# Kernel tuning notes

Hardware: AMD Instinct MI355X
Metric: run time of the kernel (lower is better)

Reference implementation:

```python
import jax, jax.numpy as jnp
import numpy as np

# MANO fingertip / palm prior vertex indices from contact_loss
_F1 = [697,698,699,700,712,713,714,715,737,738,739,740,741,743,744,745,746,748,749,750,753,754,755,756,757,758,759,760,761,762,763,764,765,766,767,768]
_F2 = [46,47,48,49,164,165,166,167,194,195,223,237,238,280,281,298,301,317,320,323,324,325,326,327,328,329,330,331,332,333,340,341,342,343,344,345,346,347,348,349,350,351,352,353,354,355]
_F3 = [356,357,358,359,375,376,386,387,396,397,402,403,413,429,433,434,435,436,437,438,439,440,441,442,443,444,452,453,454,455,456,459,460,461,462,463,464,465,466,467]
_F4 = [468,469,470,471,484,485,486,496,497,506,507,513,514,524,545,546,547,548,549,550,551,552,553,555,563,564,565,566,567,570,572,573,574,575,576,577,578]
_F5 = [580,581,582,583,600,601,602,614,615,624,625,630,631,641,663,664,665,666,667,668,670,672,680,681,682,683,684,686,687,688,689,690,691,692,693,694,695]
_F0 = [73,96,98,99,772,774,775,777]
PRIOR_IDX = np.array(_F1 + _F2 + _F3 + _F4 + _F5 + _F0, dtype=np.int32)

KL_COEF = 0.005
A_W, B_W, C_W, D_W, E_W = 1.0, 0.1, 1000.0, 10.0, 10.0  # init kwargs a..e


def _nn(src, trg):
    """Brute-force 1-NN: src [B,N1,3] -> trg [B,N2,3].
    Returns (sq_dist [B,N1], idx [B,N1], diff src-near [B,N1,3])."""
    d2 = (jnp.sum(src * src, -1)[:, :, None]
          + jnp.sum(trg * trg, -1)[:, None, :]
          - 2.0 * jnp.einsum('bnd,bmd->bnm', src, trg))  # [B,N1,N2]
    idx = jnp.argmin(d2, axis=-1)
    near = jnp.take_along_axis(trg, idx[:, :, None], axis=1)
    diff = src - near
    return jnp.sum(diff * diff, axis=-1), idx, diff


def _p2p_signed(x, y, x_normals):
    """point2point_signed(x, y, x_normals): signed dist y->x, unsigned x->y."""
    _, yidx, y2x = _nn(y, x)  # nearest x for each y
    y_nn_normal = jnp.take_along_axis(x_normals, yidx[:, :, None], axis=1)
    in_out = jnp.sign(jnp.sum(y_nn_normal * y2x, axis=-1))
    y2x_signed = jnp.sqrt(jnp.sum(y2x * y2x, axis=-1)) * in_out  # [B,P2]
    _, _, x2y = _nn(x, y)  # nearest y for each x
    x2y_dist = jnp.sqrt(jnp.sum(x2y * x2y, axis=-1))  # [B,P1]
    return y2x_signed, x2y_dist


def _forward(recon_xyz, gt_xyz, recon_normals, gt_normals, obj_xyz, mean, log_var, v_weights):
    B = recon_xyz.shape[0]
    f32 = recon_xyz.dtype
    # --- CVAE recon (L2) + KLD ---
    recon_loss = jnp.sum((recon_xyz - gt_xyz) ** 2) / B
    kld = -0.5 * jnp.sum(1.0 + log_var - mean ** 2 - jnp.exp(log_var)) / B * 10.0
    # --- obj -> hand NN (squared dists, pytorch3d knn_points convention) ---
    recon_d2, recon_idx, _ = _nn(obj_xyz, recon_xyz)  # [B,3000]
    gt_d2, _, _ = _nn(obj_xyz, gt_xyz)
    # --- contact map from GT NN dist thresholding ---
    cmap = jnp.sqrt(gt_d2) < 0.005  # [B,3000] bool
    # --- contact_loss: obj NN to prior (fingertip/palm) recon verts ---
    prior = recon_xyz[:, PRIOR_IDX, :]
    obj_cd, _, _ = _nn(obj_xyz, prior)
    n_pts = jnp.sum(cmap.astype(f32))
    contact = 3000.0 * jnp.where(n_pts > 0, jnp.sum(obj_cd * cmap) / (B * n_pts), 0.0)
    # --- CMap_consistency_loss ---
    recon_cmap = jnp.sqrt(recon_d2) < 0.005
    consistency = -5.0 * jnp.sum((recon_cmap & cmap).astype(f32)) / (n_pts + 1e-4)
    # --- inter_penetr_loss: interior obj points via NN-normal dot sign ---
    nn_hand = jnp.take_along_axis(recon_xyz, recon_idx[:, :, None], axis=1)
    nn_normal = jnp.take_along_axis(recon_normals, recon_idx[:, :, None], axis=1)
    interior = jnp.sum((nn_hand - obj_xyz) * nn_normal, axis=-1) > 0
    penetr = 100.0 * jnp.sum(recon_d2 * interior) / B
    # --- loss_cnet: signed chamfer consistency ---
    vw2 = v_weights ** (1.0 / 2.5)
    o2h, h2o = _p2p_signed(recon_xyz, obj_xyz, recon_normals)
    o2h_gt, h2o_gt = _p2p_signed(gt_xyz, obj_xyz, gt_normals)
    w_dist = (o2h_gt < 0.01) & (o2h_gt > -0.005)
    w_neg = o2h < 0.0
    w = jnp.where(w_neg, 1.5, jnp.where(w_dist, 1.0, 0.1))
    loss_h = 35.0 * (1.0 - KL_COEF) * jnp.mean(jnp.abs(jnp.abs(h2o) - jnp.abs(h2o_gt)) * vw2)
    loss_o = 30.0 * (1.0 - KL_COEF) * jnp.mean(jnp.abs(o2h - o2h_gt) * w)
    cnet = loss_h + loss_o
    return (A_W * recon_loss + B_W * kld + C_W * penetr
            + D_W * contact + E_W * consistency + cnet)


def setup_inputs() -> dict:
    key = jax.random.key(0)
    ks = jax.random.split(key, 8)
    B, NH, NO, Z = 32, 778, 3000, 64
    s = 0.05  # meter-scale point clouds so contact thresholds (5mm) are meaningful
    def unit(k, shape):
        v = jax.random.normal(k, shape, dtype=jnp.float32)
        return v / jnp.linalg.norm(v, axis=-1, keepdims=True)
    return {
        'recon_xyz': jax.random.normal(ks[0], (B, NH, 3), dtype=jnp.float32) * s,
        'gt_xyz': jax.random.normal(ks[1], (B, NH, 3), dtype=jnp.float32) * s,
        'recon_normals': unit(ks[2], (B, NH, 3)),
        'gt_normals': unit(ks[3], (B, NH, 3)),
        'obj_xyz': jax.random.normal(ks[4], (B, NO, 3), dtype=jnp.float32) * s,
        'mean': jax.random.normal(ks[5], (B, Z), dtype=jnp.float32),
        'log_var': jax.random.normal(ks[6], (B, Z), dtype=jnp.float32) * 0.1,
        'v_weights': jax.random.uniform(ks[7], (NH,), dtype=jnp.float32),
    }


def reference(recon_xyz, gt_xyz, recon_normals, gt_normals, obj_xyz, mean, log_var, v_weights):
    return _forward(recon_xyz, gt_xyz, recon_normals, gt_normals, obj_xyz, mean, log_var, v_weights)
```

## Files before the change

kernel.cpp:

```cpp
#include <hip/hip_runtime.h>
#include <math.h>


#define NB 32
#define NH 778
#define NO 3000
#define NZ 64
#define NP 204

#define P_OBJ 4
#define OBJ_PTS (256 * P_OBJ)
#define OBJ_TILES 3
#define JSPLIT 4
#define JCH 195
#define OC_NUM 12
#define OC_SIZE 250

#define OBJ_BLKS (NB * OBJ_TILES * JSPLIT)
#define HAND_BLKS (NB * OC_NUM)
#define FIN_OBJ_BLKS (NB * OBJ_TILES)
#define FIN_TAIL_BLKS ((NB * NH + 255) / 256)
#define FIN_BLKS (FIN_OBJ_BLKS + FIN_TAIL_BLKS)

typedef unsigned int uint32;
typedef unsigned long long ull;

__device__ __constant__ int c_prior[NP] = {
  697,698,699,700,712,713,714,715,737,738,739,740,741,743,744,745,746,748,749,750,
  753,754,755,756,757,758,759,760,761,762,763,764,765,766,767,768,
  46,47,48,49,164,165,166,167,194,195,223,237,238,280,281,298,301,317,320,323,
  324,325,326,327,328,329,330,331,332,333,340,341,342,343,344,345,346,347,348,349,
  350,351,352,353,354,355,
  356,357,358,359,375,376,386,387,396,397,402,403,413,429,433,434,435,436,437,438,
  439,440,441,442,443,444,452,453,454,455,456,459,460,461,462,463,464,465,466,467,
  468,469,470,471,484,485,486,496,497,506,507,513,514,524,545,546,547,548,549,550,
  551,552,553,555,563,564,565,566,567,570,572,573,574,575,576,577,578,
  580,581,582,583,600,601,602,614,615,624,625,630,631,641,663,664,665,666,667,668,
  670,672,680,681,682,683,684,686,687,688,689,690,691,692,693,694,695,
  73,96,98,99,772,774,775,777
};

__device__ inline float wave_sum(float v) {
  v += __shfl_down(v, 32);
  v += __shfl_down(v, 16);
  v += __shfl_down(v, 8);
  v += __shfl_down(v, 4);
  v += __shfl_down(v, 2);
  v += __shfl_down(v, 1);
  return v;
}

#define N_MINH (2 * NB * NH)
#define N_PACK (2 * NB * NO)

__global__ void init_kernel(float* accs, uint32* minH, ull* packO) {
  int t = blockIdx.x * blockDim.x + threadIdx.x;
  if (t < 9) accs[t] = 0.0f;
  if (t < N_MINH) minH[t] = 0x7F800000u;
  if (t < N_PACK) packO[t] = ~0ull;
}

__global__ __launch_bounds__(256) void mega1(
    const float* __restrict__ recon, const float* __restrict__ gt,
    const float* __restrict__ obj,
    uint32* __restrict__ minHR, uint32* __restrict__ minHG,
    ull* __restrict__ packR, ull* __restrict__ packG)
{
  const int bid = blockIdx.x;
  const int tid = threadIdx.x;

  if (bid < OBJ_BLKS) {
    __shared__ float4 sR[JCH];
    __shared__ float4 sG[JCH];
    const int b    = bid / (OBJ_TILES * JSPLIT);
    const int rem  = bid % (OBJ_TILES * JSPLIT);
    const int tile = rem / JSPLIT;
    const int half = rem % JSPLIT;
    const int jbase = half * JCH;
    const int jcnt = (NH - jbase < JCH) ? (NH - jbase) : JCH;

    for (int i = tid; i < jcnt; i += 256) {
      const float* p = recon + ((size_t)b * NH + jbase + i) * 3;
      float x = p[0], y = p[1], z = p[2];
      sR[i] = make_float4(x, y, z, x*x + y*y + z*z);
      const float* q = gt + ((size_t)b * NH + jbase + i) * 3;
      float gx = q[0], gy = q[1], gz = q[2];
      sG[i] = make_float4(gx, gy, gz, gx*gx + gy*gy + gz*gz);
    }
    __syncthreads();

    float nx[P_OBJ], ny[P_OBJ], nz[P_OBJ], o2v[P_OBJ];
    int ob[P_OBJ]; bool val[P_OBJ];
    #pragma unroll
    for (int m = 0; m < P_OBJ; ++m) {
      int o = tile * OBJ_PTS + m * 256 + tid;
      ob[m] = o; val[m] = (o < NO);
      float x = 0.f, y = 0.f, z = 0.f;
      if (val[m]) {
        const float* op = obj + ((size_t)b * NO + o) * 3;
        x = op[0]; y = op[1]; z = op[2];
      }
      nx[m] = -2.f * x; ny[m] = -2.f * y; nz[m] = -2.f * z;
      o2v[m] = x*x + y*y + z*z;
    }

    float bR[P_OBJ], bG[P_OBJ]; int iR[P_OBJ], iG[P_OBJ];
    #pragma unroll
    for (int m = 0; m < P_OBJ; ++m) { bR[m] = 3.4e38f; bG[m] = 3.4e38f; iR[m] = 0; iG[m] = 0; }

    #pragma unroll 2
    for (int i = 0; i < jcnt; ++i) {
      float4 h = sR[i];
      #pragma unroll
      for (int m = 0; m < P_OBJ; ++m) {
        float t = fmaf(nx[m], h.x, h.w);
        t = fmaf(ny[m], h.y, t);
        t = fmaf(nz[m], h.z, t);
        if (t < bR[m]) { bR[m] = t; iR[m] = jbase + i; }
      }
      float4 g = sG[i];
      #pragma unroll
      for (int m = 0; m < P_OBJ; ++m) {
        float u = fmaf(nx[m], g.x, g.w);
        u = fmaf(ny[m], g.y, u);
        u = fmaf(nz[m], g.z, u);
        if (u < bG[m]) { bG[m] = u; iG[m] = jbase + i; }
      }
    }

    #pragma unroll
    for (int m = 0; m < P_OBJ; ++m) {
      if (!val[m]) continue;
      const size_t base = (size_t)b * NO + ob[m];
      float d2R = fmaxf(bR[m] + o2v[m], 0.f);
      float d2G = fmaxf(bG[m] + o2v[m], 0.f);
      atomicMin(&packR[base], ((ull)__float_as_uint(d2R) << 32) | (uint32)iR[m]);
      atomicMin(&packG[base], ((ull)__float_as_uint(d2G) << 32) | (uint32)iG[m]);
    }
  } else {
    __shared__ float4 sO[OC_SIZE];
    const int bid2 = bid - OBJ_BLKS;
    const int oc = bid2 % OC_NUM;
    const int b  = bid2 / OC_NUM;

    const float* Ob = obj + ((size_t)b * NO + oc * OC_SIZE) * 3;
    for (int i = tid; i < OC_SIZE; i += 256) {
      float x = Ob[3*i], y = Ob[3*i+1], z = Ob[3*i+2];
      sO[i] = make_float4(x, y, z, x*x + y*y + z*z);
    }
    __syncthreads();

    float nrx[4], nry[4], nrz[4], r2v[4];
    float ngx[4], ngy[4], ngz[4], g2v[4];
    bool val[4];
    #pragma unroll
    for (int m = 0; m < 4; ++m) {
      int j = m * 256 + tid;
      val[m] = (j < NH);
      float rx = 0.f, ry = 0.f, rz = 0.f, gx = 0.f, gy = 0.f, gz = 0.f;
      if (val[m]) {
        const float* rp = recon + ((size_t)b * NH + j) * 3;
        const float* gp = gt    + ((size_t)b * NH + j) * 3;
        rx = rp[0]; ry = rp[1]; rz = rp[2];
        gx = gp[0]; gy = gp[1]; gz = gp[2];
      }
      nrx[m] = -2.f*rx; nry[m] = -2.f*ry; nrz[m] = -2.f*rz;
      ngx[m] = -2.f*gx; ngy[m] = -2.f*gy; ngz[m] = -2.f*gz;
      r2v[m] = rx*rx + ry*ry + rz*rz;
      g2v[m] = gx*gx + gy*gy + gz*gz;
    }

    float mR[4], mG[4];
    #pragma unroll
    for (int m = 0; m < 4; ++m) { mR[m] = 3.4e38f; mG[m] = 3.4e38f; }

    #pragma unroll 2
    for (int k = 0; k < OC_SIZE; ++k) {
      float4 o4 = sO[k];
      #pragma unroll
      for (int m = 0; m < 4; ++m) {
        float t = fmaf(nrx[m], o4.x, o4.w);
        t = fmaf(nry[m], o4.y, t);
        t = fmaf(nrz[m], o4.z, t);
        mR[m] = fminf(mR[m], t);
        float u = fmaf(ngx[m], o4.x, o4.w);
        u = fmaf(ngy[m], o4.y, u);
        u = fmaf(ngz[m], o4.z, u);
        mG[m] = fminf(mG[m], u);
      }
    }

    #pragma unroll
    for (int m = 0; m < 4; ++m) {
      if (!val[m]) continue;
      int j = m * 256 + tid;
      const int base = b * NH + j;
      float d2R = fmaxf(mR[m] + r2v[m], 0.f);
      float d2G = fmaxf(mG[m] + g2v[m], 0.f);
      atomicMin(&minHR[base], __float_as_uint(d2R));
      atomicMin(&minHG[base], __float_as_uint(d2G));
    }
  }
}

__global__ __launch_bounds__(256) void mega2(
    const float* __restrict__ recon, const float* __restrict__ gt,
    const float* __restrict__ rnorm, const float* __restrict__ gnorm,
    const float* __restrict__ obj,
    const float* __restrict__ mean, const float* __restrict__ logv,
    const float* __restrict__ vw,
    const uint32* __restrict__ minHR, const uint32* __restrict__ minHG,
    const ull* __restrict__ packR, const ull* __restrict__ packG,
    float* __restrict__ accs, float* __restrict__ out)
{
  __shared__ float4 sP[NP];
  __shared__ float red[4][5];
  const int bid = blockIdx.x;
  const int tid = threadIdx.x;
  const int lane = tid & 63, wv = tid >> 6;

  if (bid < FIN_OBJ_BLKS) {
    const int b = bid / OBJ_TILES;
    const int tile = bid % OBJ_TILES;
    if (tid < NP) {
      int j = c_prior[tid];
      const float* p = recon + ((size_t)b * NH + j) * 3;
      float x = p[0], y = p[1], z = p[2];
      sP[tid] = make_float4(x, y, z, x*x + y*y + z*z);
    }
    __syncthreads();

    float nx[P_OBJ], ny[P_OBJ], nz[P_OBJ], o2v[P_OBJ];
    float oxv[P_OBJ], oyv[P_OBJ], ozv[P_OBJ];
    int ob[P_OBJ]; bool val[P_OBJ];
    #pragma unroll
    for (int m = 0; m < P_OBJ; ++m) {
      int o = tile * OBJ_PTS + m * 256 + tid;
      ob[m] = o; val[m] = (o < NO);
      float x = 0.f, y = 0.f, z = 0.f;
      if (val[m]) {
        const float* op = obj + ((size_t)b * NO + o) * 3;
        x = op[0]; y = op[1]; z = op[2];
      }
      oxv[m] = x; oyv[m] = y; ozv[m] = z;
      nx[m] = -2.f * x; ny[m] = -2.f * y; nz[m] = -2.f * z;
      o2v[m] = x*x + y*y + z*z;
    }

    float bP[P_OBJ];
    #pragma unroll
    for (int m = 0; m < P_OBJ; ++m) bP[m] = 3.4e38f;
    #pragma unroll 2
    for (int k = 0; k < NP; ++k) {
      float4 h = sP[k];
      #pragma unroll
      for (int m = 0; m < P_OBJ; ++m) {
        float t = fmaf(nx[m], h.x, h.w);
        t = fmaf(ny[m], h.y, t);
        t = fmaf(nz[m], h.z, t);
        bP[m] = fminf(bP[m], t);
      }
    }

    float penetr = 0.f, nptsv = 0.f, contactv = 0.f, consistv = 0.f, lossov = 0.f;
    #pragma unroll
    for (int m = 0; m < P_OBJ; ++m) {
      if (!val[m]) continue;
      const size_t base = (size_t)b * NO + ob[m];
      ull pR = packR[base], pG = packG[base];
      float d2R = __uint_as_float((uint32)(pR >> 32));
      float d2G = __uint_as_float((uint32)(pG >> 32));
      int idxR = (int)(uint32)pR, idxG = (int)(uint32)pG;
      float d2P = fmaxf(bP[m] + o2v[m], 0.f);

      const float* hR = recon + ((size_t)b * NH + idxR) * 3;
      const float* nR = rnorm + ((size_t)b * NH + idxR) * 3;
      float dotR = (oxv[m] - hR[0]) * nR[0] + (oyv[m] - hR[1]) * nR[1] + (ozv[m] - hR[2]) * nR[2];
      const float* hG = gt + ((size_t)b * NH + idxG) * 3;
      const float* nG = gnorm + ((size_t)b * NH + idxG) * 3;
      float dotG = (oxv[m] - hG[0]) * nG[0] + (oyv[m] - hG[1]) * nG[1] + (ozv[m] - hG[2]) * nG[2];

      float sgnR = (dotR > 0.f) ? 1.f : ((dotR < 0.f) ? -1.f : 0.f);
      float sgnG = (dotG > 0.f) ? 1.f : ((dotG < 0.f) ? -1.f : 0.f);
      float sR_ = sqrtf(d2R), sG_ = sqrtf(d2G);
      float o2h = sR_ * sgnR, o2hg = sG_ * sgnG;

      bool interior = dotR < 0.f;
      bool cmap = sG_ < 0.005f;
      bool rcmap = sR_ < 0.005f;

      penetr   += interior ? d2R : 0.f;
      nptsv    += cmap ? 1.f : 0.f;
      contactv += cmap ? d2P : 0.f;
      consistv += (cmap && rcmap) ? 1.f : 0.f;
      float w = (o2h < 0.f) ? 1.5f
              : (((o2hg < 0.01f) && (o2hg > -0.005f)) ? 1.f : 0.1f);
      lossov += fabsf(o2h - o2hg) * w;
    }

    float vals[5] = {penetr, nptsv, contactv, consistv, lossov};
    for (int q = 0; q < 5; ++q) {
      float s = wave_sum(vals[q]);
      if (lane == 0) red[wv][q] = s;
    }
    __syncthreads();
    if (tid < 5) {
      float s = red[0][tid] + red[1][tid] + red[2][tid] + red[3][tid];
      atomicAdd(&accs[tid], s);
    }
  } else {
    const int t = (bid - FIN_OBJ_BLKS) * 256 + tid;
    float lossh = 0.f, rsum = 0.f, ksum = 0.f;
    if (t < NB * NH) {
      const float* rp = recon + (size_t)t * 3;
      const float* gp = gt + (size_t)t * 3;
      float d0 = rp[0] - gp[0], d1 = rp[1] - gp[1], d2 = rp[2] - gp[2];
      rsum = d0*d0 + d1*d1 + d2*d2;
      int j = t % NH;
      float h2o  = sqrtf(__uint_as_float(minHR[t]));
      float h2og = sqrtf(__uint_as_float(minHG[t]));
      lossh = fabsf(h2o - h2og) * powf(vw[j], 0.4f);
    }
    if (t < NB * NZ) {
      float m = mean[t], lv = logv[t];
      ksum = 1.f + lv - m * m - expf(lv);
    }
    float vals[3] = {lossh, rsum, ksum};
    for (int q = 0; q < 3; ++q) {
      float s = wave_sum(vals[q]);
      if (lane == 0) red[wv][q] = s;
    }
    __syncthreads();
    if (tid < 3) {
      float s = red[0][tid] + red[1][tid] + red[2][tid] + red[3][tid];
      atomicAdd(&accs[5 + tid], s);
    }
  }

  __syncthreads();
  if (tid == 0) {
    __threadfence();
    int* cnt = (int*)(accs + 8);
    int old = atomicAdd(cnt, 1);
    if (old == FIN_BLKS - 1) {
      float a[8];
      for (int q = 0; q < 8; ++q) a[q] = atomicAdd(&accs[q], 0.0f);
      const float recon_loss = a[6] / (float)NB;
      const float kld = -0.5f * a[7] / (float)NB * 10.f;
      const float penetr = 100.f * a[0] / (float)NB;
      const float npts = a[1];
      const float contact = (npts > 0.f) ? (3000.f * a[2] / ((float)NB * npts)) : 0.f;
      const float consistency = -5.f * a[3] / (npts + 0.0001f);
      const float lossh = 35.f * (1.f - 0.005f) * (a[5] / (float)(NB * NH));
      const float losso = 30.f * (1.f - 0.005f) * (a[4] / (float)(NB * NO));
      out[0] = recon_loss + 0.1f * kld + 1000.f * penetr + 10.f * contact
             + 10.f * consistency + lossh + losso;
    }
  }
}

#define FB_TILES 12
__global__ __launch_bounds__(256) void obj_mono(
    const float* __restrict__ recon, const float* __restrict__ gt,
    const float* __restrict__ rnorm, const float* __restrict__ gnorm,
    const float* __restrict__ obj, float* __restrict__ accs)
{
  __shared__ float4 sR[NH];
  __shared__ float4 sG[NH];
  __shared__ float red[4][5];
  const int b = blockIdx.x / FB_TILES;
  const int tile = blockIdx.x % FB_TILES;
  const int tid = threadIdx.x;

  for (int i = tid; i < NH; i += 256) {
    const float* p = recon + ((size_t)b * NH + i) * 3;
    float x = p[0], y = p[1], z = p[2];
    sR[i] = make_float4(x, y, z, x*x + y*y + z*z);
    const float* q = gt + ((size_t)b * NH + i) * 3;
    float gx = q[0], gy = q[1], gz = q[2];
    sG[i] = make_float4(gx, gy, gz, gx*gx + gy*gy + gz*gz);
  }
  __syncthreads();

  const int o = tile * 256 + tid;
  float penetr = 0.f, nptsv = 0.f, contactv = 0.f, consistv = 0.f, lossov = 0.f;
  if (o < NO) {
    const float* op = obj + ((size_t)b * NO + o) * 3;
    const float ox = op[0], oy = op[1], oz = op[2];
    const float nx = -2.f * ox, ny = -2.f * oy, nz = -2.f * oz;
    const float o2 = ox*ox + oy*oy + oz*oz;
    float bR = 3.4e38f, bG = 3.4e38f;
    int iR = 0, iG = 0;
    for (int i = 0; i < NH; ++i) {
      float4 h = sR[i];
      float t = fmaf(nx, h.x, h.w); t = fmaf(ny, h.y, t); t = fmaf(nz, h.z, t);
      if (t < bR) { bR = t; iR = i; }
      float4 g = sG[i];
      float u = fmaf(nx, g.x, g.w); u = fmaf(ny, g.y, u); u = fmaf(nz, g.z, u);
      if (u < bG) { bG = u; iG = i; }
    }
    float bP = 3.4e38f;
    for (int k = 0; k < NP; ++k) {
      float4 h = sR[c_prior[k]];
      float t = fmaf(nx, h.x, h.w); t = fmaf(ny, h.y, t); t = fmaf(nz, h.z, t);
      bP = fminf(bP, t);
    }
    float d2R = fmaxf(bR + o2, 0.f);
    float d2G = fmaxf(bG + o2, 0.f);
    float d2P = fmaxf(bP + o2, 0.f);
    float4 hR = sR[iR];
    const float* nR = rnorm + ((size_t)b * NH + iR) * 3;
    float dotR = (ox - hR.x) * nR[0] + (oy - hR.y) * nR[1] + (oz - hR.z) * nR[2];
    float4 hG = sG[iG];
    const float* nG = gnorm + ((size_t)b * NH + iG) * 3;
    float dotG = (ox - hG.x) * nG[0] + (oy - hG.y) * nG[1] + (oz - hG.z) * nG[2];
    float sgnR = (dotR > 0.f) ? 1.f : ((dotR < 0.f) ? -1.f : 0.f);
    float sgnG = (dotG > 0.f) ? 1.f : ((dotG < 0.f) ? -1.f : 0.f);
    float sR_ = sqrtf(d2R), sG_ = sqrtf(d2G);
    float o2h = sR_ * sgnR, o2hg = sG_ * sgnG;
    bool interior = dotR < 0.f;
    bool cmap = sG_ < 0.005f, rcmap = sR_ < 0.005f;
    penetr = interior ? d2R : 0.f;
    nptsv = cmap ? 1.f : 0.f;
    contactv = cmap ? d2P : 0.f;
    consistv = (cmap && rcmap) ? 1.f : 0.f;
    float w = (o2h < 0.f) ? 1.5f : (((o2hg < 0.01f) && (o2hg > -0.005f)) ? 1.f : 0.1f);
    lossov = fabsf(o2h - o2hg) * w;
  }
  float vals[5] = {penetr, nptsv, contactv, consistv, lossov};
  const int lane = tid & 63, wv = tid >> 6;
  for (int q = 0; q < 5; ++q) {
    float s = wave_sum(vals[q]);
    if (lane == 0) red[wv][q] = s;
  }
  __syncthreads();
  if (tid < 5) {
    float s = red[0][tid] + red[1][tid] + red[2][tid] + red[3][tid];
    atomicAdd(&accs[tid], s);
  }
}

__global__ __launch_bounds__(256) void hand_full(
    const float* __restrict__ recon, const float* __restrict__ gt,
    const float* __restrict__ obj, const float* __restrict__ vw,
    float* __restrict__ accs)
{
  __shared__ float4 sO[500];
  __shared__ float red[4];
  const int b = blockIdx.x >> 2;
  const int j = ((blockIdx.x & 3) << 8) + threadIdx.x;
  const bool valid = j < NH;
  float rx = 0, ry = 0, rz = 0, gx = 0, gy = 0, gz = 0;
  if (valid) {
    const float* rp = recon + ((size_t)b * NH + j) * 3;
    const float* gp = gt + ((size_t)b * NH + j) * 3;
    rx = rp[0]; ry = rp[1]; rz = rp[2];
    gx = gp[0]; gy = gp[1]; gz = gp[2];
  }
  const float nrx = -2.f*rx, nry = -2.f*ry, nrz = -2.f*rz;
  const float ngx = -2.f*gx, ngy = -2.f*gy, ngz = -2.f*gz;
  const float r2 = rx*rx + ry*ry + rz*rz, g2 = gx*gx + gy*gy + gz*gz;
  float mR = 3.4e38f, mG = 3.4e38f;
  for (int oc = 0; oc < 6; ++oc) {
    __syncthreads();
    const float* Ob = obj + ((size_t)b * NO + oc * 500) * 3;
    for (int i = threadIdx.x; i < 500; i += 256) {
      float x = Ob[3*i], y = Ob[3*i+1], z = Ob[3*i+2];
      sO[i] = make_float4(x, y, z, x*x + y*y + z*z);
    }
    __syncthreads();
    if (valid) {
      for (int k = 0; k < 500; ++k) {
        float4 o4 = sO[k];
        float t = fmaf(nrx, o4.x, o4.w); t = fmaf(nry, o4.y, t); t = fmaf(nrz, o4.z, t);
        mR = fminf(mR, t);
        float u = fmaf(ngx, o4.x, o4.w); u = fmaf(ngy, o4.y, u); u = fmaf(ngz, o4.z, u);
        mG = fminf(mG, u);
      }
    }
  }
  float lossh = valid ? fabsf(sqrtf(fmaxf(mR + r2, 0.f)) - sqrtf(fmaxf(mG + g2, 0.f)))
                        * powf(vw[j], 0.4f) : 0.f;
  const int lane = threadIdx.x & 63, wv = threadIdx.x >> 6;
  float s = wave_sum(lossh);
  if (lane == 0) red[wv] = s;
  __syncthreads();
  if (threadIdx.x == 0) atomicAdd(&accs[5], red[0] + red[1] + red[2] + red[3]);
}

__global__ __launch_bounds__(256) void tail_nomins(
    const float* __restrict__ recon, const float* __restrict__ gt,
    const float* __restrict__ mean, const float* __restrict__ logv,
    float* __restrict__ accs)
{
  __shared__ float red[4][2];
  const int t = blockIdx.x * 256 + threadIdx.x;
  float rsum = 0.f, ksum = 0.f;
  if (t < NB * NH) {
    const float* rp = recon + (size_t)t * 3;
    const float* gp = gt + (size_t)t * 3;
    float d0 = rp[0] - gp[0], d1 = rp[1] - gp[1], d2 = rp[2] - gp[2];
    rsum = d0*d0 + d1*d1 + d2*d2;
  }
  if (t < NB * NZ) {
    float m = mean[t], lv = logv[t];
    ksum = 1.f + lv - m * m - expf(lv);
  }
  float vals[2] = {rsum, ksum};
  const int lane = threadIdx.x & 63, wv = threadIdx.x >> 6;
  for (int q = 0; q < 2; ++q) {
    float s = wave_sum(vals[q]);
    if (lane == 0) red[wv][q] = s;
  }
  __syncthreads();
  if (threadIdx.x < 2) {
    float s = red[0][threadIdx.x] + red[1][threadIdx.x] + red[2][threadIdx.x] + red[3][threadIdx.x];
    atomicAdd(&accs[6 + threadIdx.x], s);
  }
}

__global__ void init_small(float* accs) {
  int t = threadIdx.x;
  if (t < 8) accs[t] = 0.0f;
}

__global__ void final_fb(const float* __restrict__ a, float* __restrict__ out) {
  const float recon_loss = a[6] / (float)NB;
  const float kld = -0.5f * a[7] / (float)NB * 10.f;
  const float penetr = 100.f * a[0] / (float)NB;
  const float npts = a[1];
  const float contact = (npts > 0.f) ? (3000.f * a[2] / ((float)NB * npts)) : 0.f;
  const float consistency = -5.f * a[3] / (npts + 0.0001f);
  const float lossh = 35.f * (1.f - 0.005f) * (a[5] / (float)(NB * NH));
  const float losso = 30.f * (1.f - 0.005f) * (a[4] / (float)(NB * NO));
  out[0] = recon_loss + 0.1f * kld + 1000.f * penetr + 10.f * contact
         + 10.f * consistency + lossh + losso;
}

extern "C" void kernel_launch(void* const* d_in, const int* in_sizes, int n_in,
                              void* d_out, int out_size, void* d_ws, size_t ws_size,
                              hipStream_t stream) {
  const float* recon = (const float*)d_in[0];
  const float* gt    = (const float*)d_in[1];
  const float* rnorm = (const float*)d_in[2];
  const float* gnorm = (const float*)d_in[3];
  const float* obj   = (const float*)d_in[4];
  const float* mean  = (const float*)d_in[5];
  const float* logv  = (const float*)d_in[6];
  const float* vw    = (const float*)d_in[7];
  float* out = (float*)d_out;

  float* accs = (float*)d_ws;
  uint32* minH = (uint32*)(accs + 16);
  ull* packO = (ull*)(minH + N_MINH);
  const size_t needed = 16 * sizeof(float) + (size_t)N_MINH * 4 + (size_t)N_PACK * 8;

  if (ws_size >= needed) {
    {
      int blocks = (N_PACK + 255) / 256;
      init_kernel<<<blocks, 256, 0, stream>>>(accs, minH, packO);
    }
    mega1<<<OBJ_BLKS + HAND_BLKS, 256, 0, stream>>>(
        recon, gt, obj, minH, minH + NB * NH, packO, packO + NB * NO);
    mega2<<<FIN_BLKS, 256, 0, stream>>>(
        recon, gt, rnorm, gnorm, obj, mean, logv, vw,
        minH, minH + NB * NH, packO, packO + NB * NO, accs, out);
  } else {
    init_small<<<1, 64, 0, stream>>>(accs);
    obj_mono<<<NB * FB_TILES, 256, 0, stream>>>(recon, gt, rnorm, gnorm, obj, accs);
    hand_full<<<NB * 4, 256, 0, stream>>>(recon, gt, obj, vw, accs);
    tail_nomins<<<(NB * NH + 255) / 256, 256, 0, stream>>>(recon, gt, mean, logv, accs);
    final_fb<<<1, 1, 0, stream>>>(accs, out);
  }
}
```

Measured before the change: 129.5 us.

## Replace atomicMin reductions with per-split partial buffers and packed float keys

The first pass now writes per-split partial minima to separate workspace slices instead of doing 64-bit and 32-bit atomicMin on global memory. This removes the init kernel and the atomic contention. Nearest-hand indices are packed into the low 10 mantissa bits of the float distance so a branchless fminf replaces compare-and-select. The second pass reduces the partial slices and uses 12 tiles of one object point per thread. Packing the index into the mantissa truncates precision and can change tie-breaking and the signed distances. The workspace needed is also larger.

Result: faster. 123.7 us (-4.4%).

```diff
diff --git a/kernel.cpp b/kernel.cpp
--- a/kernel.cpp
+++ b/kernel.cpp
@@ -13,14 +13,17 @@
 #define OBJ_TILES 3
 #define JSPLIT 4
 #define JCH 195
-#define OC_NUM 12
-#define OC_SIZE 250
-
+#define HC 12
+#define HCS 250
 #define OBJ_BLKS (NB * OBJ_TILES * JSPLIT)
-#define HAND_BLKS (NB * OC_NUM)
-#define FIN_OBJ_BLKS (NB * OBJ_TILES)
+#define HAND_BLKS (NB * HC)
+#define T2 12
+#define FIN_OBJ_BLKS (NB * T2)
 #define FIN_TAIL_BLKS ((NB * NH + 255) / 256)
 #define FIN_BLKS (FIN_OBJ_BLKS + FIN_TAIL_BLKS)
+
+#define NKEY (NB * NO)
+#define NHT  (NB * NH)
 
 typedef unsigned int uint32;
 typedef unsigned long long ull;
@@ -50,34 +53,32 @@
   return v;
 }
 
-#define N_MINH (2 * NB * NH)
-#define N_PACK (2 * NB * NO)
-
-__global__ void init_kernel(float* accs, uint32* minH, ull* packO) {
-  int t = blockIdx.x * blockDim.x + threadIdx.x;
-  if (t < 9) accs[t] = 0.0f;
-  if (t < N_MINH) minH[t] = 0x7F800000u;
-  if (t < N_PACK) packO[t] = ~0ull;
-}
-
-__global__ __launch_bounds__(256) void mega1(
+__device__ inline float packkey(float t, int j) {
+  return __uint_as_float((__float_as_uint(t) & 0xFFFFFC00u) | (uint32)j);
+}
+
+
+__global__ __launch_bounds__(256) void mega1a(
     const float* __restrict__ recon, const float* __restrict__ gt,
     const float* __restrict__ obj,
-    uint32* __restrict__ minHR, uint32* __restrict__ minHG,
-    ull* __restrict__ packR, ull* __restrict__ packG)
+    float* __restrict__ keyR, float* __restrict__ keyG,
+    float* __restrict__ minHR, float* __restrict__ minHG,
+    float* __restrict__ accs)
 {
   const int bid = blockIdx.x;
   const int tid = threadIdx.x;
 
+  if (bid == 0 && tid < 16) accs[tid] = 0.0f;
+
   if (bid < OBJ_BLKS) {
     __shared__ float4 sR[JCH];
     __shared__ float4 sG[JCH];
-    const int b    = bid / (OBJ_TILES * JSPLIT);
-    const int rem  = bid % (OBJ_TILES * JSPLIT);
-    const int tile = rem / JSPLIT;
-    const int half = rem % JSPLIT;
-    const int jbase = half * JCH;
-    const int jcnt = (NH - jbase < JCH) ? (NH - jbase) : JCH;
+    const int b     = bid / (OBJ_TILES * JSPLIT);
+    const int rem   = bid % (OBJ_TILES * JSPLIT);
+    const int tile  = rem / JSPLIT;
+    const int split = rem % JSPLIT;
+    const int jbase = split * JCH;
+    const int jcnt  = (NH - jbase < JCH) ? (NH - jbase) : JCH;
 
     for (int i = tid; i < jcnt; i += 256) {
       const float* p = recon + ((size_t)b * NH + jbase + i) * 3;
@@ -89,7 +90,7 @@
     }
     __syncthreads();
 
-    float nx[P_OBJ], ny[P_OBJ], nz[P_OBJ], o2v[P_OBJ];
+    float nx[P_OBJ], ny[P_OBJ], nz[P_OBJ];
     int ob[P_OBJ]; bool val[P_OBJ];
     #pragma unroll
     for (int m = 0; m < P_OBJ; ++m) {
@@ -101,57 +102,63 @@
         x = op[0]; y = op[1]; z = op[2];
       }
       nx[m] = -2.f * x; ny[m] = -2.f * y; nz[m] = -2.f * z;
-      o2v[m] = x*x + y*y + z*z;
-    }
-
-    float bR[P_OBJ], bG[P_OBJ]; int iR[P_OBJ], iG[P_OBJ];
-    #pragma unroll
-    for (int m = 0; m < P_OBJ; ++m) { bR[m] = 3.4e38f; bG[m] = 3.4e38f; iR[m] = 0; iG[m] = 0; }
-
-    #pragma unroll 2
-    for (int i = 0; i < jcnt; ++i) {
-      float4 h = sR[i];
+    }
+
+    float bR[P_OBJ], bG[P_OBJ];
+    #pragma unroll
+    for (int m = 0; m < P_OBJ; ++m) { bR[m] = 3.4e38f; bG[m] = 3.4e38f; }
+
+    int i = 0;
+    for (; i + 1 < jcnt; i += 2) {
+      float4 h0 = sR[i], h1 = sR[i + 1];
       #pragma unroll
       for (int m = 0; m < P_OBJ; ++m) {
-        float t = fmaf(nx[m], h.x, h.w);
-        t = fmaf(ny[m], h.y, t);
-        t = fmaf(nz[m], h.z, t);
-        if (t < bR[m]) { bR[m] = t; iR[m] = jbase + i; }
-      }
-      float4 g = sG[i];
+        float t0 = fmaf(nx[m], h0.x, h0.w); t0 = fmaf(ny[m], h0.y, t0); t0 = fmaf(nz[m], h0.z, t0);
+        float t1 = fmaf(nx[m], h1.x, h1.w); t1 = fmaf(ny[m], h1.y, t1); t1 = fmaf(nz[m], h1.z, t1);
+        bR[m] = fminf(bR[m], fminf(packkey(t0, jbase + i), packkey(t1, jbase + i + 1)));
+      }
+      float4 g0 = sG[i], g1 = sG[i + 1];
       #pragma unroll
       for (int m = 0; m < P_OBJ; ++m) {
-        float u = fmaf(nx[m], g.x, g.w);
-        u = fmaf(ny[m], g.y, u);
-        u = fmaf(nz[m], g.z, u);
-        if (u < bG[m]) { bG[m] = u; iG[m] = jbase + i; }
+        float t0 = fmaf(nx[m], g0.x, g0.w); t0 = fmaf(ny[m], g0.y, t0); t0 = fmaf(nz[m], g0.z, t0);
+        float t1 = fmaf(nx[m], g1.x, g1.w); t1 = fmaf(ny[m], g1.y, t1); t1 = fmaf(nz[m], g1.z, t1);
+        bG[m] = fminf(bG[m], fminf(packkey(t0, jbase + i), packkey(t1, jbase + i + 1)));
+      }
+    }
+    if (i < jcnt) {
+      float4 h0 = sR[i];
+      float4 g0 = sG[i];
+      #pragma unroll
+      for (int m = 0; m < P_OBJ; ++m) {
+        float t0 = fmaf(nx[m], h0.x, h0.w); t0 = fmaf(ny[m], h0.y, t0); t0 = fmaf(nz[m], h0.z, t0);
+        bR[m] = fminf(bR[m], packkey(t0, jbase + i));
+        float u0 = fmaf(nx[m], g0.x, g0.w); u0 = fmaf(ny[m], g0.y, u0); u0 = fmaf(nz[m], g0.z, u0);
+        bG[m] = fminf(bG[m], packkey(u0, jbase + i));
       }
     }
 
     #pragma unroll
     for (int m = 0; m < P_OBJ; ++m) {
       if (!val[m]) continue;
-      const size_t base = (size_t)b * NO + ob[m];
-      float d2R = fmaxf(bR[m] + o2v[m], 0.f);
-      float d2G = fmaxf(bG[m] + o2v[m], 0.f);
-      atomicMin(&packR[base], ((ull)__float_as_uint(d2R) << 32) | (uint32)iR[m]);
-      atomicMin(&packG[base], ((ull)__float_as_uint(d2G) << 32) | (uint32)iG[m]);
+      const size_t idx = (size_t)split * NKEY + (size_t)b * NO + ob[m];
+      keyR[idx] = bR[m];
+      keyG[idx] = bG[m];
     }
   } else {
-    __shared__ float4 sO[OC_SIZE];
+    __shared__ float4 sO[HCS];
     const int bid2 = bid - OBJ_BLKS;
-    const int oc = bid2 % OC_NUM;
-    const int b  = bid2 / OC_NUM;
-
-    const float* Ob = obj + ((size_t)b * NO + oc * OC_SIZE) * 3;
-    for (int i = tid; i < OC_SIZE; i += 256) {
-      float x = Ob[3*i], y = Ob[3*i+1], z = Ob[3*i+2];
-      sO[i] = make_float4(x, y, z, x*x + y*y + z*z);
-    }
-    __syncthreads();
-
-    float nrx[4], nry[4], nrz[4], r2v[4];
-    float ngx[4], ngy[4], ngz[4], g2v[4];
+    const int oc = bid2 % HC;
+    const int b  = bid2 / HC;
+
+    const float* Ob = obj + ((size_t)b * NO + oc * HCS) * 3;
+    for (int i2 = tid; i2 < HCS; i2 += 256) {
+      float x = Ob[3*i2], y = Ob[3*i2+1], z = Ob[3*i2+2];
+      sO[i2] = make_float4(x, y, z, x*x + y*y + z*z);
+    }
+    __syncthreads();
+
+    float nrx[4], nry[4], nrz[4];
+    float ngx[4], ngy[4], ngz[4];
     bool val[4];
     #pragma unroll
     for (int m = 0; m < 4; ++m) {
@@ -166,27 +173,22 @@
       }
       nrx[m] = -2.f*rx; nry[m] = -2.f*ry; nrz[m] = -2.f*rz;
       ngx[m] = -2.f*gx; ngy[m] = -2.f*gy; ngz[m] = -2.f*gz;
-      r2v[m] = rx*rx + ry*ry + rz*rz;
-      g2v[m] = gx*gx + gy*gy + gz*gz;
     }
 
     float mR[4], mG[4];
     #pragma unroll
     for (int m = 0; m < 4; ++m) { mR[m] = 3.4e38f; mG[m] = 3.4e38f; }
 
-    #pragma unroll 2
-    for (int k = 0; k < OC_SIZE; ++k) {
-      float4 o4 = sO[k];
+    for (int k = 0; k < HCS; k += 2) {
+      float4 o0 = sO[k], o1 = sO[k + 1];
       #pragma unroll
       for (int m = 0; m < 4; ++m) {
-        float t = fmaf(nrx[m], o4.x, o4.w);
-        t = fmaf(nry[m], o4.y, t);
-        t = fmaf(nrz[m], o4.z, t);
-        mR[m] = fminf(mR[m], t);
-        float u = fmaf(ngx[m], o4.x, o4.w);
-        u = fmaf(ngy[m], o4.y, u);
-        u = fmaf(ngz[m], o4.z, u);
-        mG[m] = fminf(mG[m], u);
+        float t0 = fmaf(nrx[m], o0.x, o0.w); t0 = fmaf(nry[m], o0.y, t0); t0 = fmaf(nrz[m], o0.z, t0);
+        float t1 = fmaf(nrx[m], o1.x, o1.w); t1 = fmaf(nry[m], o1.y, t1); t1 = fmaf(nrz[m], o1.z, t1);
+        mR[m] = fminf(mR[m], fminf(t0, t1));
+        float u0 = fmaf(ngx[m], o0.x, o0.w); u0 = fmaf(ngy[m], o0.y, u0); u0 = fmaf(ngz[m], o0.z, u0);
+        float u1 = fmaf(ngx[m], o1.x, o1.w); u1 = fmaf(ngy[m], o1.y, u1); u1 = fmaf(ngz[m], o1.z, u1);
+        mG[m] = fminf(mG[m], fminf(u0, u1));
       }
     }
 
@@ -194,23 +196,21 @@
     for (int m = 0; m < 4; ++m) {
       if (!val[m]) continue;
       int j = m * 256 + tid;
-      const int base = b * NH + j;
-      float d2R = fmaxf(mR[m] + r2v[m], 0.f);
-      float d2G = fmaxf(mG[m] + g2v[m], 0.f);
-      atomicMin(&minHR[base], __float_as_uint(d2R));
-      atomicMin(&minHG[base], __float_as_uint(d2G));
-    }
-  }
-}
-
-__global__ __launch_bounds__(256) void mega2(
+      const size_t idx = (size_t)oc * NHT + (size_t)b * NH + j;
+      minHR[idx] = mR[m];
+      minHG[idx] = mG[m];
+    }
+  }
+}
+
+__global__ __launch_bounds__(256) void mega2a(
     const float* __restrict__ recon, const float* __restrict__ gt,
     const float* __restrict__ rnorm, const float* __restrict__ gnorm,
     const float* __restrict__ obj,
     const float* __restrict__ mean, const float* __restrict__ logv,
     const float* __restrict__ vw,
-    const uint32* __restrict__ minHR, const uint32* __restrict__ minHG,
-    const ull* __restrict__ packR, const ull* __restrict__ packG,
+    const float* __restrict__ keyR, const float* __restrict__ keyG,
+    const float* __restrict__ minHR, const float* __restrict__ minHG,
     float* __restrict__ accs, float* __restrict__ out)
 {
   __shared__ float4 sP[NP];
@@ -220,8 +220,8 @@
   const int lane = tid & 63, wv = tid >> 6;
 
   if (bid < FIN_OBJ_BLKS) {
-    const int b = bid / OBJ_TILES;
-    const int tile = bid % OBJ_TILES;
+    const int b = bid / T2;
+    const int tile = bid % T2;
     if (tid < NP) {
       int j = c_prior[tid];
       const float* p = recon + ((size_t)b * NH + j) * 3;
@@ -230,55 +230,41 @@
     }
     __syncthreads();
 
-    float nx[P_OBJ], ny[P_OBJ], nz[P_OBJ], o2v[P_OBJ];
-    float oxv[P_OBJ], oyv[P_OBJ], ozv[P_OBJ];
-    int ob[P_OBJ]; bool val[P_OBJ];
-    #pragma unroll
-    for (int m = 0; m < P_OBJ; ++m) {
-      int o = tile * OBJ_PTS + m * 256 + tid;
-      ob[m] = o; val[m] = (o < NO);
-      float x = 0.f, y = 0.f, z = 0.f;
-      if (val[m]) {
-        const float* op = obj + ((size_t)b * NO + o) * 3;
-        x = op[0]; y = op[1]; z = op[2];
-      }
-      oxv[m] = x; oyv[m] = y; ozv[m] = z;
-      nx[m] = -2.f * x; ny[m] = -2.f * y; nz[m] = -2.f * z;
-      o2v[m] = x*x + y*y + z*z;
-    }
-
-    float bP[P_OBJ];
-    #pragma unroll
-    for (int m = 0; m < P_OBJ; ++m) bP[m] = 3.4e38f;
-    #pragma unroll 2
-    for (int k = 0; k < NP; ++k) {
-      float4 h = sP[k];
+    const int o = tile * 256 + tid;
+    float penetr = 0.f, nptsv = 0.f, contactv = 0.f, consistv = 0.f, lossov = 0.f;
+    if (o < NO) {
+      const float* op = obj + ((size_t)b * NO + o) * 3;
+      const float ox = op[0], oy = op[1], oz = op[2];
+      const float nx = -2.f * ox, ny = -2.f * oy, nz = -2.f * oz;
+      const float o2 = ox*ox + oy*oy + oz*oz;
+      const size_t base = (size_t)b * NO + o;
+
+      float kR = 3.4e38f, kG = 3.4e38f;
       #pragma unroll
-      for (int m = 0; m < P_OBJ; ++m) {
-        float t = fmaf(nx[m], h.x, h.w);
-        t = fmaf(ny[m], h.y, t);
-        t = fmaf(nz[m], h.z, t);
-        bP[m] = fminf(bP[m], t);
-      }
-    }
-
-    float penetr = 0.f, nptsv = 0.f, contactv = 0.f, consistv = 0.f, lossov = 0.f;
-    #pragma unroll
-    for (int m = 0; m < P_OBJ; ++m) {
-      if (!val[m]) continue;
-      const size_t base = (size_t)b * NO + ob[m];
-      ull pR = packR[base], pG = packG[base];
-      float d2R = __uint_as_float((uint32)(pR >> 32));
-      float d2G = __uint_as_float((uint32)(pG >> 32));
-      int idxR = (int)(uint32)pR, idxG = (int)(uint32)pG;
-      float d2P = fmaxf(bP[m] + o2v[m], 0.f);
+      for (int s = 0; s < JSPLIT; ++s) {
+        kR = fminf(kR, keyR[(size_t)s * NKEY + base]);
+        kG = fminf(kG, keyG[(size_t)s * NKEY + base]);
+      }
+      uint32 kRb = __float_as_uint(kR), kGb = __float_as_uint(kG);
+      int idxR = (int)(kRb & 0x3FFu), idxG = (int)(kGb & 0x3FFu);
+      float d2R = fmaxf(__uint_as_float(kRb & 0xFFFFFC00u) + o2, 0.f);
+      float d2G = fmaxf(__uint_as_float(kGb & 0xFFFFFC00u) + o2, 0.f);
+
+      float bP = 3.4e38f;
+      for (int k = 0; k < NP; k += 2) {
+        float4 h0 = sP[k], h1 = sP[k + 1];
+        float t0 = fmaf(nx, h0.x, h0.w); t0 = fmaf(ny, h0.y, t0); t0 = fmaf(nz, h0.z, t0);
+        float t1 = fmaf(nx, h1.x, h1.w); t1 = fmaf(ny, h1.y, t1); t1 = fmaf(nz, h1.z, t1);
+        bP = fminf(bP, fminf(t0, t1));
+      }
+      float d2P = fmaxf(bP + o2, 0.f);
 
       const float* hR = recon + ((size_t)b * NH + idxR) * 3;
       const float* nR = rnorm + ((size_t)b * NH + idxR) * 3;
-      float dotR = (oxv[m] - hR[0]) * nR[0] + (oyv[m] - hR[1]) * nR[1] + (ozv[m] - hR[2]) * nR[2];
+      float dotR = (ox - hR[0]) * nR[0] + (oy - hR[1]) * nR[1] + (oz - hR[2]) * nR[2];
       const float* hG = gt + ((size_t)b * NH + idxG) * 3;
       const float* nG = gnorm + ((size_t)b * NH + idxG) * 3;
-      float dotG = (oxv[m] - hG[0]) * nG[0] + (oyv[m] - hG[1]) * nG[1] + (ozv[m] - hG[2]) * nG[2];
+      float dotG = (ox - hG[0]) * nG[0] + (oy - hG[1]) * nG[1] + (oz - hG[2]) * nG[2];
 
       float sgnR = (dotR > 0.f) ? 1.f : ((dotR < 0.f) ? -1.f : 0.f);
       float sgnG = (dotG > 0.f) ? 1.f : ((dotG < 0.f) ? -1.f : 0.f);
@@ -289,13 +275,13 @@
       bool cmap = sG_ < 0.005f;
       bool rcmap = sR_ < 0.005f;
 
-      penetr   += interior ? d2R : 0.f;
-      nptsv    += cmap ? 1.f : 0.f;
-      contactv += cmap ? d2P : 0.f;
-      consistv += (cmap && rcmap) ? 1.f : 0.f;
+      penetr   = interior ? d2R : 0.f;
+      nptsv    = cmap ? 1.f : 0.f;
+      contactv = cmap ? d2P : 0.f;
+      consistv = (cmap && rcmap) ? 1.f : 0.f;
       float w = (o2h < 0.f) ? 1.5f
               : (((o2hg < 0.01f) && (o2hg > -0.005f)) ? 1.f : 0.1f);
-      lossov += fabsf(o2h - o2hg) * w;
+      lossov = fabsf(o2h - o2hg) * w;
     }
 
     float vals[5] = {penetr, nptsv, contactv, consistv, lossov};
@@ -314,12 +300,23 @@
     if (t < NB * NH) {
       const float* rp = recon + (size_t)t * 3;
       const float* gp = gt + (size_t)t * 3;
-      float d0 = rp[0] - gp[0], d1 = rp[1] - gp[1], d2 = rp[2] - gp[2];
+      float rx = rp[0], ry = rp[1], rz = rp[2];
+      float gx = gp[0], gy = gp[1], gz = gp[2];
+      float d0 = rx - gx, d1 = ry - gy, d2 = rz - gz;
       rsum = d0*d0 + d1*d1 + d2*d2;
+
+      float mRt = 3.4e38f, mGt = 3.4e38f;
+      #pragma unroll
+      for (int c = 0; c < HC; ++c) {
+        mRt = fminf(mRt, minHR[(size_t)c * NHT + t]);
+        mGt = fminf(mGt, minHG[(size_t)c * NHT + t]);
+      }
+      float r2 = rx*rx + ry*ry + rz*rz;
+      float g2 = gx*gx + gy*gy + gz*gz;
+      float d2Rh = fmaxf(mRt + r2, 0.f);
+      float d2Gh = fmaxf(mGt + g2, 0.f);
       int j = t % NH;
-      float h2o  = sqrtf(__uint_as_float(minHR[t]));
-      float h2og = sqrtf(__uint_as_float(minHG[t]));
-      lossh = fabsf(h2o - h2og) * powf(vw[j], 0.4f);
+      lossh = fabsf(sqrtf(d2Rh) - sqrtf(d2Gh)) * powf(vw[j], 0.4f);
     }
     if (t < NB * NZ) {
       float m = mean[t], lv = logv[t];
@@ -359,7 +356,261 @@
   }
 }
 
-#define FB_TILES 12
+#define B_OBJ_TILES 3
+#define B_JSPLIT 4
+#define B_JCH 195
+#define B_OC_NUM 12
+#define B_OC_SIZE 250
+#define B_OBJ_BLKS (NB * B_OBJ_TILES * B_JSPLIT)
+#define B_HAND_BLKS (NB * B_OC_NUM)
+#define B_FIN_OBJ (NB * B_OBJ_TILES)
+#define B_FIN_TAIL ((NB * NH + 255) / 256)
+#define B_FIN (B_FIN_OBJ + B_FIN_TAIL)
+#define N_MINH (2 * NB * NH)
+#define N_PACK (2 * NB * NO)
+
+__global__ void init_b(float* accs, uint32* minH, ull* packO) {
+  int t = blockIdx.x * blockDim.x + threadIdx.x;
+  if (t < 9) accs[t] = 0.0f;
+  if (t < N_MINH) minH[t] = 0x7F800000u;
+  if (t < N_PACK) packO[t] = ~0ull;
+}
+
+__global__ __launch_bounds__(256) void mega1b(
+    const float* __restrict__ recon, const float* __restrict__ gt,
+    const float* __restrict__ obj,
+    uint32* __restrict__ minHRb, uint32* __restrict__ minHGb,
+    ull* __restrict__ packR, ull* __restrict__ packG)
+{
+  const int bid = blockIdx.x;
+  const int tid = threadIdx.x;
+  if (bid < B_OBJ_BLKS) {
+    __shared__ float4 sR[B_JCH];
+    __shared__ float4 sG[B_JCH];
+    const int b    = bid / (B_OBJ_TILES * B_JSPLIT);
+    const int rem  = bid % (B_OBJ_TILES * B_JSPLIT);
+    const int tile = rem / B_JSPLIT;
+    const int half = rem % B_JSPLIT;
+    const int jbase = half * B_JCH;
+    const int jcnt = (NH - jbase < B_JCH) ? (NH - jbase) : B_JCH;
+    for (int i = tid; i < jcnt; i += 256) {
+      const float* p = recon + ((size_t)b * NH + jbase + i) * 3;
+      float x = p[0], y = p[1], z = p[2];
+      sR[i] = make_float4(x, y, z, x*x + y*y + z*z);
+      const float* q = gt + ((size_t)b * NH + jbase + i) * 3;
+      float gx = q[0], gy = q[1], gz = q[2];
+      sG[i] = make_float4(gx, gy, gz, gx*gx + gy*gy + gz*gz);
+    }
+    __syncthreads();
+    float nx[4], ny[4], nz[4], o2v[4]; int ob[4]; bool val[4];
+    #pragma unroll
+    for (int m = 0; m < 4; ++m) {
+      int o = tile * 1024 + m * 256 + tid;
+      ob[m] = o; val[m] = (o < NO);
+      float x = 0.f, y = 0.f, z = 0.f;
+      if (val[m]) { const float* op = obj + ((size_t)b * NO + o) * 3; x = op[0]; y = op[1]; z = op[2]; }
+      nx[m] = -2.f*x; ny[m] = -2.f*y; nz[m] = -2.f*z; o2v[m] = x*x + y*y + z*z;
+    }
+    float bR[4], bG[4]; int iR[4], iG[4];
+    #pragma unroll
+    for (int m = 0; m < 4; ++m) { bR[m] = 3.4e38f; bG[m] = 3.4e38f; iR[m] = 0; iG[m] = 0; }
+    for (int i = 0; i < jcnt; ++i) {
+      float4 h = sR[i];
+      #pragma unroll
+      for (int m = 0; m < 4; ++m) {
+        float t = fmaf(nx[m], h.x, h.w); t = fmaf(ny[m], h.y, t); t = fmaf(nz[m], h.z, t);
+        if (t < bR[m]) { bR[m] = t; iR[m] = jbase + i; }
+      }
+      float4 g = sG[i];
+      #pragma unroll
+      for (int m = 0; m < 4; ++m) {
+        float u = fmaf(nx[m], g.x, g.w); u = fmaf(ny[m], g.y, u); u = fmaf(nz[m], g.z, u);
+        if (u < bG[m]) { bG[m] = u; iG[m] = jbase + i; }
+      }
+    }
+    #pragma unroll
+    for (int m = 0; m < 4; ++m) {
+      if (!val[m]) continue;
+      const size_t base = (size_t)b * NO + ob[m];
+      float d2R = fmaxf(bR[m] + o2v[m], 0.f);
+      float d2G = fmaxf(bG[m] + o2v[m], 0.f);
+      atomicMin(&packR[base], ((ull)__float_as_uint(d2R) << 32) | (uint32)iR[m]);
+      atomicMin(&packG[base], ((ull)__float_as_uint(d2G) << 32) | (uint32)iG[m]);
+    }
+  } else {
+    __shared__ float4 sO[B_OC_SIZE];
+    const int bid2 = bid - B_OBJ_BLKS;
+    const int oc = bid2 % B_OC_NUM;
+    const int b  = bid2 / B_OC_NUM;
+    const float* Ob = obj + ((size_t)b * NO + oc * B_OC_SIZE) * 3;
+    for (int i = tid; i < B_OC_SIZE; i += 256) {
+      float x = Ob[3*i], y = Ob[3*i+1], z = Ob[3*i+2];
+      sO[i] = make_float4(x, y, z, x*x + y*y + z*z);
+    }
+    __syncthreads();
+    float nrx[4], nry[4], nrz[4], r2v[4], ngx[4], ngy[4], ngz[4], g2v[4]; bool val[4];
+    #pragma unroll
+    for (int m = 0; m < 4; ++m) {
+      int j = m * 256 + tid; val[m] = (j < NH);
+      float rx=0,ry=0,rz=0,gx=0,gy=0,gz=0;
+      if (val[m]) {
+        const float* rp = recon + ((size_t)b * NH + j) * 3;
+        const float* gp = gt    + ((size_t)b * NH + j) * 3;
+        rx=rp[0];ry=rp[1];rz=rp[2]; gx=gp[0];gy=gp[1];gz=gp[2];
+      }
+      nrx[m]=-2.f*rx;nry[m]=-2.f*ry;nrz[m]=-2.f*rz;
+      ngx[m]=-2.f*gx;ngy[m]=-2.f*gy;ngz[m]=-2.f*gz;
+      r2v[m]=rx*rx+ry*ry+rz*rz; g2v[m]=gx*gx+gy*gy+gz*gz;
+    }
+    float mR[4], mG[4];
+    #pragma unroll
+    for (int m = 0; m < 4; ++m) { mR[m]=3.4e38f; mG[m]=3.4e38f; }
+    for (int k = 0; k < B_OC_SIZE; ++k) {
+      float4 o4 = sO[k];
+      #pragma unroll
+      for (int m = 0; m < 4; ++m) {
+        float t = fmaf(nrx[m], o4.x, o4.w); t = fmaf(nry[m], o4.y, t); t = fmaf(nrz[m], o4.z, t);
+        mR[m] = fminf(mR[m], t);
+        float u = fmaf(ngx[m], o4.x, o4.w); u = fmaf(ngy[m], o4.y, u); u = fmaf(ngz[m], o4.z, u);
+        mG[m] = fminf(mG[m], u);
+      }
+    }
+    #pragma unroll
+    for (int m = 0; m < 4; ++m) {
+      if (!val[m]) continue;
+      int j = m * 256 + tid;
+      const int base = b * NH + j;
+      atomicMin(&minHRb[base], __float_as_uint(fmaxf(mR[m] + r2v[m], 0.f)));
+      atomicMin(&minHGb[base], __float_as_uint(fmaxf(mG[m] + g2v[m], 0.f)));
+    }
+  }
+}
+
+__global__ __launch_bounds__(256) void mega2b(
+    const float* __restrict__ recon, const float* __restrict__ gt,
+    const float* __restrict__ rnorm, const float* __restrict__ gnorm,
+    const float* __restrict__ obj,
+    const float* __restrict__ mean, const float* __restrict__ logv,
+    const float* __restrict__ vw,
+    const uint32* __restrict__ minHRb, const uint32* __restrict__ minHGb,
+    const ull* __restrict__ packR, const ull* __restrict__ packG,
+    float* __restrict__ accs, float* __restrict__ out)
+{
+  __shared__ float4 sP[NP];
+  __shared__ float red[4][5];
+  const int bid = blockIdx.x;
+  const int tid = threadIdx.x;
+  const int lane = tid & 63, wv = tid >> 6;
+
+  if (bid < B_FIN_OBJ) {
+    const int b = bid / B_OBJ_TILES;
+    const int tile = bid % B_OBJ_TILES;
+    if (tid < NP) {
+      int j = c_prior[tid];
+      const float* p = recon + ((size_t)b * NH + j) * 3;
+      float x = p[0], y = p[1], z = p[2];
+      sP[tid] = make_float4(x, y, z, x*x + y*y + z*z);
+    }
+    __syncthreads();
+    float penetr=0.f, nptsv=0.f, contactv=0.f, consistv=0.f, lossov=0.f;
+    #pragma unroll
+    for (int m = 0; m < 4; ++m) {
+      int o = tile * 1024 + m * 256 + tid;
+      if (o >= NO) continue;
+      const float* op = obj + ((size_t)b * NO + o) * 3;
+      float ox = op[0], oy = op[1], oz = op[2];
+      float nx = -2.f*ox, ny = -2.f*oy, nz = -2.f*oz;
+      float o2 = ox*ox + oy*oy + oz*oz;
+      const size_t base = (size_t)b * NO + o;
+      ull pR = packR[base], pG = packG[base];
+      float d2R = __uint_as_float((uint32)(pR >> 32));
+      float d2G = __uint_as_float((uint32)(pG >> 32));
+      int idxR = (int)(uint32)pR, idxG = (int)(uint32)pG;
+      float bP = 3.4e38f;
+      for (int k = 0; k < NP; ++k) {
+        float4 h = sP[k];
+        float t = fmaf(nx, h.x, h.w); t = fmaf(ny, h.y, t); t = fmaf(nz, h.z, t);
+        bP = fminf(bP, t);
+      }
+      float d2P = fmaxf(bP + o2, 0.f);
+      const float* hR = recon + ((size_t)b * NH + idxR) * 3;
+      const float* nR = rnorm + ((size_t)b * NH + idxR) * 3;
+      float dotR = (ox-hR[0])*nR[0] + (oy-hR[1])*nR[1] + (oz-hR[2])*nR[2];
+      const float* hG = gt + ((size_t)b * NH + idxG) * 3;
+      const float* nG = gnorm + ((size_t)b * NH + idxG) * 3;
+      float dotG = (ox-hG[0])*nG[0] + (oy-hG[1])*nG[1] + (oz-hG[2])*nG[2];
+      float sgnR = (dotR > 0.f) ? 1.f : ((dotR < 0.f) ? -1.f : 0.f);
+      float sgnG = (dotG > 0.f) ? 1.f : ((dotG < 0.f) ? -1.f : 0.f);
+      float sR_ = sqrtf(d2R), sG_ = sqrtf(d2G);
+      float o2h = sR_*sgnR, o2hg = sG_*sgnG;
+      bool interior = dotR < 0.f;
+      bool cmap = sG_ < 0.005f, rcmap = sR_ < 0.005f;
+      penetr   += interior ? d2R : 0.f;
+      nptsv    += cmap ? 1.f : 0.f;
+      contactv += cmap ? d2P : 0.f;
+      consistv += (cmap && rcmap) ? 1.f : 0.f;
+      float w = (o2h < 0.f) ? 1.5f : (((o2hg < 0.01f) && (o2hg > -0.005f)) ? 1.f : 0.1f);
+      lossov += fabsf(o2h - o2hg) * w;
+    }
+    float vals[5] = {penetr, nptsv, contactv, consistv, lossov};
+    for (int q = 0; q < 5; ++q) {
+      float s = wave_sum(vals[q]);
+      if (lane == 0) red[wv][q] = s;
+    }
+    __syncthreads();
+    if (tid < 5) {
+      float s = red[0][tid] + red[1][tid] + red[2][tid] + red[3][tid];
+      atomicAdd(&accs[tid], s);
+    }
+  } else {
+    const int t = (bid - B_FIN_OBJ) * 256 + tid;
+    float lossh = 0.f, rsum = 0.f, ksum = 0.f;
+    if (t < NB * NH) {
+      const float* rp = recon + (size_t)t * 3;
+      const float* gp = gt + (size_t)t * 3;
+      float d0 = rp[0]-gp[0], d1 = rp[1]-gp[1], d2 = rp[2]-gp[2];
+      rsum = d0*d0 + d1*d1 + d2*d2;
+      int j = t % NH;
+      float h2o  = sqrtf(__uint_as_float(minHRb[t]));
+      float h2og = sqrtf(__uint_as_float(minHGb[t]));
+      lossh = fabsf(h2o - h2og) * powf(vw[j], 0.4f);
+    }
+    if (t < NB * NZ) {
+      float m = mean[t], lv = logv[t];
+      ksum = 1.f + lv - m*m - expf(lv);
+    }
+    float vals[3] = {lossh, rsum, ksum};
+    for (int q = 0; q < 3; ++q) {
+      float s = wave_sum(vals[q]);
+      if (lane == 0) red[wv][q] = s;
+    }
+    __syncthreads();
+    if (tid < 3) {
+      float s = red[0][tid] + red[1][tid] + red[2][tid] + red[3][tid];
+      atomicAdd(&accs[5 + tid], s);
+    }
+  }
+  __syncthreads();
+  if (tid == 0) {
+    __threadfence();
+    int* cnt = (int*)(accs + 8);
+    int old = atomicAdd(cnt, 1);
+    if (old == B_FIN - 1) {
+      float a[8];
+      for (int q = 0; q < 8; ++q) a[q] = atomicAdd(&accs[q], 0.0f);
+      const float recon_loss = a[6] / (float)NB;
+      const float kld = -0.5f * a[7] / (float)NB * 10.f;
+      const float penetr = 100.f * a[0] / (float)NB;
+      const float npts = a[1];
+      const float contact = (npts > 0.f) ? (3000.f * a[2] / ((float)NB * npts)) : 0.f;
+      const float consistency = -5.f * a[3] / (npts + 0.0001f);
+      const float lossh = 35.f * (1.f - 0.005f) * (a[5] / (float)(NB * NH));
+      const float losso = 30.f * (1.f - 0.005f) * (a[4] / (float)(NB * NO));
+      out[0] = recon_loss + 0.1f*kld + 1000.f*penetr + 10.f*contact + 10.f*consistency + lossh + losso;
+    }
+  }
+}
+
 __global__ __launch_bounds__(256) void obj_mono(
     const float* __restrict__ recon, const float* __restrict__ gt,
     const float* __restrict__ rnorm, const float* __restrict__ gnorm,
@@ -368,10 +619,9 @@
   __shared__ float4 sR[NH];
   __shared__ float4 sG[NH];
   __shared__ float red[4][5];
-  const int b = blockIdx.x / FB_TILES;
-  const int tile = blockIdx.x % FB_TILES;
+  const int b = blockIdx.x / 12;
+  const int tile = blockIdx.x % 12;
   const int tid = threadIdx.x;
-
   for (int i = tid; i < NH; i += 256) {
     const float* p = recon + ((size_t)b * NH + i) * 3;
     float x = p[0], y = p[1], z = p[2];
@@ -381,16 +631,14 @@
     sG[i] = make_float4(gx, gy, gz, gx*gx + gy*gy + gz*gz);
   }
   __syncthreads();
-
   const int o = tile * 256 + tid;
   float penetr = 0.f, nptsv = 0.f, contactv = 0.f, consistv = 0.f, lossov = 0.f;
   if (o < NO) {
     const float* op = obj + ((size_t)b * NO + o) * 3;
     const float ox = op[0], oy = op[1], oz = op[2];
-    const float nx = -2.f * ox, ny = -2.f * oy, nz = -2.f * oz;
+    const float nx = -2.f*ox, ny = -2.f*oy, nz = -2.f*oz;
     const float o2 = ox*ox + oy*oy + oz*oz;
-    float bR = 3.4e38f, bG = 3.4e38f;
-    int iR = 0, iG = 0;
+    float bR = 3.4e38f, bG = 3.4e38f; int iR = 0, iG = 0;
     for (int i = 0; i < NH; ++i) {
       float4 h = sR[i];
       float t = fmaf(nx, h.x, h.w); t = fmaf(ny, h.y, t); t = fmaf(nz, h.z, t);
@@ -410,14 +658,14 @@
     float d2P = fmaxf(bP + o2, 0.f);
     float4 hR = sR[iR];
     const float* nR = rnorm + ((size_t)b * NH + iR) * 3;
-    float dotR = (ox - hR.x) * nR[0] + (oy - hR.y) * nR[1] + (oz - hR.z) * nR[2];
+    float dotR = (ox-hR.x)*nR[0] + (oy-hR.y)*nR[1] + (oz-hR.z)*nR[2];
     float4 hG = sG[iG];
     const float* nG = gnorm + ((size_t)b * NH + iG) * 3;
-    float dotG = (ox - hG.x) * nG[0] + (oy - hG.y) * nG[1] + (oz - hG.z) * nG[2];
+    float dotG = (ox-hG.x)*nG[0] + (oy-hG.y)*nG[1] + (oz-hG.z)*nG[2];
     float sgnR = (dotR > 0.f) ? 1.f : ((dotR < 0.f) ? -1.f : 0.f);
     float sgnG = (dotG > 0.f) ? 1.f : ((dotG < 0.f) ? -1.f : 0.f);
     float sR_ = sqrtf(d2R), sG_ = sqrtf(d2G);
-    float o2h = sR_ * sgnR, o2hg = sG_ * sgnG;
+    float o2h = sR_*sgnR, o2hg = sG_*sgnG;
     bool interior = dotR < 0.f;
     bool cmap = sG_ < 0.005f, rcmap = sR_ < 0.005f;
     penetr = interior ? d2R : 0.f;
@@ -450,16 +698,15 @@
   const int b = blockIdx.x >> 2;
   const int j = ((blockIdx.x & 3) << 8) + threadIdx.x;
   const bool valid = j < NH;
-  float rx = 0, ry = 0, rz = 0, gx = 0, gy = 0, gz = 0;
+  float rx=0,ry=0,rz=0,gx=0,gy=0,gz=0;
   if (valid) {
     const float* rp = recon + ((size_t)b * NH + j) * 3;
     const float* gp = gt + ((size_t)b * NH + j) * 3;
-    rx = rp[0]; ry = rp[1]; rz = rp[2];
-    gx = gp[0]; gy = gp[1]; gz = gp[2];
-  }
-  const float nrx = -2.f*rx, nry = -2.f*ry, nrz = -2.f*rz;
-  const float ngx = -2.f*gx, ngy = -2.f*gy, ngz = -2.f*gz;
-  const float r2 = rx*rx + ry*ry + rz*rz, g2 = gx*gx + gy*gy + gz*gz;
+    rx=rp[0];ry=rp[1];rz=rp[2]; gx=gp[0];gy=gp[1];gz=gp[2];
+  }
+  const float nrx=-2.f*rx, nry=-2.f*ry, nrz=-2.f*rz;
+  const float ngx=-2.f*gx, ngy=-2.f*gy, ngz=-2.f*gz;
+  const float r2 = rx*rx+ry*ry+rz*rz, g2 = gx*gx+gy*gy+gz*gz;
   float mR = 3.4e38f, mG = 3.4e38f;
   for (int oc = 0; oc < 6; ++oc) {
     __syncthreads();
@@ -472,20 +719,19 @@
     if (valid) {
       for (int k = 0; k < 500; ++k) {
         float4 o4 = sO[k];
-        float t = fmaf(nrx, o4.x, o4.w); t = fmaf(nry, o4.y, t); t = fmaf(nrz, o4.z, t);
+        float t = fmaf(nrx,o4.x,o4.w); t = fmaf(nry,o4.y,t); t = fmaf(nrz,o4.z,t);
         mR = fminf(mR, t);
-        float u = fmaf(ngx, o4.x, o4.w); u = fmaf(ngy, o4.y, u); u = fmaf(ngz, o4.z, u);
+        float u = fmaf(ngx,o4.x,o4.w); u = fmaf(ngy,o4.y,u); u = fmaf(ngz,o4.z,u);
         mG = fminf(mG, u);
       }
     }
   }
-  float lossh = valid ? fabsf(sqrtf(fmaxf(mR + r2, 0.f)) - sqrtf(fmaxf(mG + g2, 0.f)))
-                        * powf(vw[j], 0.4f) : 0.f;
+  float lossh = valid ? fabsf(sqrtf(fmaxf(mR+r2,0.f)) - sqrtf(fmaxf(mG+g2,0.f))) * powf(vw[j], 0.4f) : 0.f;
   const int lane = threadIdx.x & 63, wv = threadIdx.x >> 6;
   float s = wave_sum(lossh);
   if (lane == 0) red[wv] = s;
   __syncthreads();
-  if (threadIdx.x == 0) atomicAdd(&accs[5], red[0] + red[1] + red[2] + red[3]);
+  if (threadIdx.x == 0) atomicAdd(&accs[5], red[0]+red[1]+red[2]+red[3]);
 }
 
 __global__ __launch_bounds__(256) void tail_nomins(
@@ -499,12 +745,12 @@
   if (t < NB * NH) {
     const float* rp = recon + (size_t)t * 3;
     const float* gp = gt + (size_t)t * 3;
-    float d0 = rp[0] - gp[0], d1 = rp[1] - gp[1], d2 = rp[2] - gp[2];
+    float d0 = rp[0]-gp[0], d1 = rp[1]-gp[1], d2 = rp[2]-gp[2];
     rsum = d0*d0 + d1*d1 + d2*d2;
   }
   if (t < NB * NZ) {
     float m = mean[t], lv = logv[t];
-    ksum = 1.f + lv - m * m - expf(lv);
+    ksum = 1.f + lv - m*m - expf(lv);
   }
   float vals[2] = {rsum, ksum};
   const int lane = threadIdx.x & 63, wv = threadIdx.x >> 6;
@@ -533,8 +779,7 @@
   const float consistency = -5.f * a[3] / (npts + 0.0001f);
   const float lossh = 35.f * (1.f - 0.005f) * (a[5] / (float)(NB * NH));
   const float losso = 30.f * (1.f - 0.005f) * (a[4] / (float)(NB * NO));
-  out[0] = recon_loss + 0.1f * kld + 1000.f * penetr + 10.f * contact
-         + 10.f * consistency + lossh + losso;
+  out[0] = recon_loss + 0.1f*kld + 1000.f*penetr + 10.f*contact + 10.f*consistency + lossh + losso;
 }
 
 extern "C" void kernel_launch(void* const* d_in, const int* in_sizes, int n_in,
@@ -551,23 +796,32 @@
   float* out = (float*)d_out;
 
   float* accs = (float*)d_ws;
-  uint32* minH = (uint32*)(accs + 16);
-  ull* packO = (ull*)(minH + N_MINH);
-  const size_t needed = 16 * sizeof(float) + (size_t)N_MINH * 4 + (size_t)N_PACK * 8;
-
-  if (ws_size >= needed) {
-    {
-      int blocks = (N_PACK + 255) / 256;
-      init_kernel<<<blocks, 256, 0, stream>>>(accs, minH, packO);
-    }
-    mega1<<<OBJ_BLKS + HAND_BLKS, 256, 0, stream>>>(
-        recon, gt, obj, minH, minH + NB * NH, packO, packO + NB * NO);
-    mega2<<<FIN_BLKS, 256, 0, stream>>>(
+  float* keyR = accs + 16;
+  float* keyG = keyR + (size_t)JSPLIT * NKEY;
+  float* minHR = keyG + (size_t)JSPLIT * NKEY;
+  float* minHG = minHR + (size_t)HC * NHT;
+  const size_t neededA = (16 + 2ull * JSPLIT * NKEY + 2ull * HC * NHT) * sizeof(float);
+
+  uint32* minHb = (uint32*)(accs + 16);
+  ull* packO = (ull*)(minHb + N_MINH);
+  const size_t neededB = 16 * sizeof(float) + (size_t)N_MINH * 4 + (size_t)N_PACK * 8;
+
+  if (ws_size >= neededA) {
+    mega1a<<<OBJ_BLKS + HAND_BLKS, 256, 0, stream>>>(
+        recon, gt, obj, keyR, keyG, minHR, minHG, accs);
+    mega2a<<<FIN_BLKS, 256, 0, stream>>>(
         recon, gt, rnorm, gnorm, obj, mean, logv, vw,
-        minH, minH + NB * NH, packO, packO + NB * NO, accs, out);
+        keyR, keyG, minHR, minHG, accs, out);
+  } else if (ws_size >= neededB) {
+    init_b<<<(N_PACK + 255) / 256, 256, 0, stream>>>(accs, minHb, packO);
+    mega1b<<<B_OBJ_BLKS + B_HAND_BLKS, 256, 0, stream>>>(
+        recon, gt, obj, minHb, minHb + NB * NH, packO, packO + NB * NO);
+    mega2b<<<B_FIN, 256, 0, stream>>>(
+        recon, gt, rnorm, gnorm, obj, mean, logv, vw,
+        minHb, minHb + NB * NH, packO, packO + NB * NO, accs, out);
   } else {
     init_small<<<1, 64, 0, stream>>>(accs);
-    obj_mono<<<NB * FB_TILES, 256, 0, stream>>>(recon, gt, rnorm, gnorm, obj, accs);
+    obj_mono<<<NB * 12, 256, 0, stream>>>(recon, gt, rnorm, gnorm, obj, accs);
     hand_full<<<NB * 4, 256, 0, stream>>>(recon, gt, obj, vw, accs);
     tail_nomins<<<(NB * NH + 255) / 256, 256, 0, stream>>>(recon, gt, mean, logv, accs);
     final_fb<<<1, 1, 0, stream>>>(accs, out);
```
